# Kernel optimization log

Hardware: AMD Instinct MI355X
Metric: run time of the kernel (lower is better)

## Reference

```python
import jax, jax.numpy as jnp
import numpy as np

B, S, IN, OUT, SPLIT = 4, 2048, 4096, 4096, 1024


def setup_inputs() -> dict:
    key = jax.random.key(0)
    ks = jax.random.split(key, 14)
    def n(k, shape, scale=1.0):
        return jax.random.normal(k, shape, dtype=jnp.float32) * scale
    return {
        "x": n(ks[0], (B, S, IN)),
        "V": n(ks[1], (SPLIT, IN)),
        "U": n(ks[2], (OUT, SPLIT)),
        "v2": n(ks[3], (1, IN), 0.05),
        "v1": n(ks[4], (1, SPLIT), 0.05),
        "u2": n(ks[5], (1, SPLIT), 0.05),
        "u1": n(ks[6], (1, OUT), 0.05),
        "V_R": n(ks[7], (SPLIT, IN)),
        "U_R": n(ks[8], (OUT, SPLIT)),
        "v2_R": n(ks[9], (1, IN), 0.05),
        "v1_R": n(ks[10], (1, SPLIT), 0.05),
        "u2_R": n(ks[11], (1, SPLIT), 0.05),
        "u1_R": n(ks[12], (1, OUT), 0.05),
        "bias": n(ks[13], (OUT,), 0.02),
    }


def _quantize(w):
    # ITQ binarization: sign(w) with straight-through estimator semantics
    return w + jax.lax.stop_gradient(jnp.sign(w) - w)


def _compute_forward(x2d, V, U, v2, v1, u2, u1):
    # x2d: [T, in]; V: [split, in]; U: [out, split]
    Vq = _quantize(V)
    Uq = _quantize(U)
    v1u2 = v1 * u2  # [1, split]
    h = (x2d * v2) @ Vq.T          # [T, split]
    return (h * v1u2) @ Uq.T * u1  # [T, out]


def reference(x, V, U, v2, v1, u2, u1, V_R, U_R, v2_R, v1_R, u2_R, u1_R, bias):
    lead = x.shape[:-1]
    x2d = x.reshape(-1, x.shape[-1])
    y = _compute_forward(x2d, V, U, v2, v1, u2, u1)
    y = y + _compute_forward(x2d, V_R, U_R, v2_R, v1_R, u2_R, u1_R)
    y = y + bias
    return y.reshape(lead + (U.shape[0],))
```

## Files before the change

### kernel.cpp

```cpp
#include <hip/hip_runtime.h>


typedef __bf16 bf16x8 __attribute__((ext_vector_type(8)));
typedef float floatx4 __attribute__((ext_vector_type(4)));

__device__ __forceinline__ unsigned short f2bf_rne(float f) {
    union { float f; unsigned u; } v; v.f = f;
    unsigned r = v.u + 0x7FFFu + ((v.u >> 16) & 1u);
    return (unsigned short)(r >> 16);
}

__device__ __forceinline__ float sgnf(float w) {
    return (float)((w > 0.f) - (w < 0.f));
}

__device__ __forceinline__ void async_copy16(const void* g, void* l) {
    __builtin_amdgcn_global_load_lds(
        (const __attribute__((address_space(1))) void*)g,
        (__attribute__((address_space(3))) void*)l, 16, 0, 0);
}


__global__ void cast_x_kernel(const float* __restrict__ x,
                              unsigned short* __restrict__ xb, int n4) {
    int i = blockIdx.x * blockDim.x + threadIdx.x;
    if (i >= n4) return;
    float4 v = ((const float4*)x)[i];
    ushort4 o;
    o.x = f2bf_rne(v.x); o.y = f2bf_rne(v.y);
    o.z = f2bf_rne(v.z); o.w = f2bf_rne(v.w);
    ((ushort4*)xb)[i] = o;
}

__global__ void prep_w_kernel(const float* __restrict__ V, const float* __restrict__ V_R,
                              const float* __restrict__ v2, const float* __restrict__ v2_R,
                              const float* __restrict__ U, const float* __restrict__ U_R,
                              const float* __restrict__ v1, const float* __restrict__ v1_R,
                              const float* __restrict__ u2, const float* __restrict__ u2_R,
                              const float* __restrict__ u1, const float* __restrict__ u1_R,
                              unsigned short* __restrict__ W1,
                              unsigned short* __restrict__ W2) {
    int bid = blockIdx.x;
    if (bid < 8192) {
        int i = bid * blockDim.x + threadIdx.x;
        int idx = i << 2;
        int scat = idx >> 12;
        int k = idx & 4095;
        const float* Vp; const float* sp;
        if (scat < 1024) { Vp = V + ((size_t)scat << 12); sp = v2; }
        else             { Vp = V_R + ((size_t)(scat - 1024) << 12); sp = v2_R; }
        float4 w = *(const float4*)(Vp + k);
        float4 s = *(const float4*)(sp + k);
        ushort4 o;
        o.x = f2bf_rne(sgnf(w.x) * s.x);
        o.y = f2bf_rne(sgnf(w.y) * s.y);
        o.z = f2bf_rne(sgnf(w.z) * s.z);
        o.w = f2bf_rne(sgnf(w.w) * s.w);
        ((ushort4*)W1)[i] = o;
    } else {
        int i = (bid - 8192) * blockDim.x + threadIdx.x;
        int idx = i << 2;
        int o = idx >> 11;
        int scat = idx & 2047;
        int branch = scat >> 10;
        int s = scat & 1023;
        const float* Up  = branch ? U_R  : U;
        const float* v1p = branch ? v1_R : v1;
        const float* u2p = branch ? u2_R : u2;
        float u1v = (branch ? u1_R : u1)[o];
        float4 w = *(const float4*)(Up + ((size_t)o << 10) + s);
        float4 a = *(const float4*)(v1p + s);
        float4 b = *(const float4*)(u2p + s);
        ushort4 out;
        out.x = f2bf_rne(sgnf(w.x) * a.x * b.x * u1v);
        out.y = f2bf_rne(sgnf(w.y) * a.y * b.y * u1v);
        out.z = f2bf_rne(sgnf(w.z) * a.z * b.z * u1v);
        out.w = f2bf_rne(sgnf(w.w) * a.w * b.w * u1v);
        ((ushort4*)W2)[i] = out;
    }
}


template <bool OUT_BF16, bool ADD_BIAS>
__global__ void gemm_bt(const unsigned short* __restrict__ A,
                        const unsigned short* __restrict__ B,
                        void* __restrict__ Cv,
                        const float* __restrict__ bias,
                        int M, int N, int K) {
    __shared__ __align__(16) unsigned short As[128 * 64];
    __shared__ __align__(16) unsigned short Bs[128 * 64];

    const int tid = threadIdx.x;
    const int wave = tid >> 6;
    const int lane = tid & 63;
    const int m0 = blockIdx.x * 128;
    const int n0 = blockIdx.y * 128;

    const int lrow = lane >> 3;
    const int lcol = (((lane & 7) ^ lrow)) << 3;

    const int wm = (wave >> 1) << 6;
    const int wn = (wave & 1) << 6;
    const int fm = lane & 15;
    const int rk = lane & 7;
    const int cgl = lane >> 4;

    floatx4 acc[4][4];
#pragma unroll
    for (int i = 0; i < 4; ++i)
#pragma unroll
        for (int j = 0; j < 4; ++j)
#pragma unroll
            for (int r = 0; r < 4; ++r) acc[i][j][r] = 0.f;

    const size_t Ks = (size_t)K;
    for (int k0 = 0; k0 < K; k0 += 64) {
#pragma unroll
        for (int i = 0; i < 4; ++i) {
            const int row = wave * 32 + i * 8;
            const unsigned short* gA = A + (size_t)(m0 + row + lrow) * Ks + (k0 + lcol);
            const unsigned short* gB = B + (size_t)(n0 + row + lrow) * Ks + (k0 + lcol);
            async_copy16(gA, &As[row * 64]);
            async_copy16(gB, &Bs[row * 64]);
        }
        __syncthreads();
#pragma unroll
        for (int ks = 0; ks < 64; ks += 32) {
            const int cg = (ks >> 3) | cgl;
            const int roff = (cg ^ rk) << 3;
            bf16x8 af[4], bfr[4];
#pragma unroll
            for (int i = 0; i < 4; ++i)
                af[i] = *(const bf16x8*)&As[(wm + i * 16 + fm) * 64 + roff];
#pragma unroll
            for (int i = 0; i < 4; ++i)
                bfr[i] = *(const bf16x8*)&Bs[(wn + i * 16 + fm) * 64 + roff];
#pragma unroll
            for (int mi = 0; mi < 4; ++mi)
#pragma unroll
                for (int ni = 0; ni < 4; ++ni)
                    acc[mi][ni] = __builtin_amdgcn_mfma_f32_16x16x32_bf16(
                        af[mi], bfr[ni], acc[mi][ni], 0, 0, 0);
        }
        __syncthreads();
    }

    const int rq = (lane >> 4) << 2;
    const int col = lane & 15;
#pragma unroll
    for (int mi = 0; mi < 4; ++mi) {
#pragma unroll
        for (int r = 0; r < 4; ++r) {
            const int gm = m0 + wm + mi * 16 + rq + r;
            const size_t base = (size_t)gm * (size_t)N;
#pragma unroll
            for (int ni = 0; ni < 4; ++ni) {
                const int gn = n0 + wn + ni * 16 + col;
                float v = acc[mi][ni][r];
                if (ADD_BIAS) v += bias[gn];
                if (OUT_BF16)
                    ((unsigned short*)Cv)[base + gn] = f2bf_rne(v);
                else
                    ((float*)Cv)[base + gn] = v;
            }
        }
    }
}


extern "C" void kernel_launch(void* const* d_in, const int* in_sizes, int n_in,
                              void* d_out, int out_size, void* d_ws, size_t ws_size,
                              hipStream_t stream) {
    const float* x    = (const float*)d_in[0];
    const float* V    = (const float*)d_in[1];
    const float* U    = (const float*)d_in[2];
    const float* v2   = (const float*)d_in[3];
    const float* v1   = (const float*)d_in[4];
    const float* u2   = (const float*)d_in[5];
    const float* u1   = (const float*)d_in[6];
    const float* V_R  = (const float*)d_in[7];
    const float* U_R  = (const float*)d_in[8];
    const float* v2_R = (const float*)d_in[9];
    const float* v1_R = (const float*)d_in[10];
    const float* u2_R = (const float*)d_in[11];
    const float* u1_R = (const float*)d_in[12];
    const float* bias = (const float*)d_in[13];
    float* out = (float*)d_out;

    char* ws = (char*)d_ws;
    unsigned short* Xb = (unsigned short*)ws;
    unsigned short* W1 = (unsigned short*)(ws + (size_t)67108864);
    unsigned short* W2 = (unsigned short*)(ws + (size_t)67108864 + 16777216);
    unsigned short* H  = (unsigned short*)(ws + (size_t)67108864 + 33554432);

    cast_x_kernel<<<32768, 256, 0, stream>>>(x, Xb, 8388608);
    prep_w_kernel<<<16384, 256, 0, stream>>>(V, V_R, v2, v2_R,
                                             U, U_R, v1, v1_R, u2, u2_R, u1, u1_R,
                                             W1, W2);

    gemm_bt<true, false><<<dim3(64, 16), 256, 0, stream>>>(Xb, W1, (void*)H, nullptr, 8192, 2048, 4096);
    gemm_bt<false, true><<<dim3(64, 32), 256, 0, stream>>>(H, W2, (void*)out, bias, 8192, 4096, 2048);
}
```

Before: 549.4 us.

## Replace GEMM with 256x256 double-buffered, software-pipelined MFMA kernel

Replaces the 128x128 single-buffered GEMM with a 256x256 tile kernel of 8 waves. It double-buffers LDS, interleaves the async global-to-LDS loads with MFMA quadrants using fine-grained vmcnt waits and barriers, and raises MFMA priority with setprio. It also remaps block IDs with a swizzle for L2 locality. The goal is to hide load latency behind compute and raise arithmetic intensity per tile. The cost is 128KB of LDS per block and high register pressure, which limits occupancy.

```diff
diff --git a/kernel.cpp b/kernel.cpp
--- a/kernel.cpp
+++ b/kernel.cpp
@@ -19,6 +19,10 @@
         (const __attribute__((address_space(1))) void*)g,
         (__attribute__((address_space(3))) void*)l, 16, 0, 0);
 }
+
+#define FENCE() asm volatile("" ::: "memory")
+#define BAR() do { FENCE(); __builtin_amdgcn_s_barrier(); FENCE(); } while (0)
+#define VMW(N) asm volatile("s_waitcnt vmcnt(" #N ")" ::: "memory")
 
 
 __global__ void cast_x_kernel(const float* __restrict__ x,
@@ -82,80 +86,153 @@
 
 
 template <bool OUT_BF16, bool ADD_BIAS>
-__global__ void gemm_bt(const unsigned short* __restrict__ A,
-                        const unsigned short* __restrict__ B,
-                        void* __restrict__ Cv,
-                        const float* __restrict__ bias,
-                        int M, int N, int K) {
-    __shared__ __align__(16) unsigned short As[128 * 64];
-    __shared__ __align__(16) unsigned short Bs[128 * 64];
+__global__ __launch_bounds__(512, 2)
+void gemm256(const unsigned short* __restrict__ A,
+             const unsigned short* __restrict__ B,
+             void* __restrict__ Cv,
+             const float* __restrict__ bias,
+             int M, int N, int K, int ntn) {
+    (void)M;
+    __shared__ __align__(16) unsigned short As[2][256 * 64];
+    __shared__ __align__(16) unsigned short Bs[2][256 * 64];
 
     const int tid = threadIdx.x;
+    const int lane = tid & 63;
     const int wave = tid >> 6;
-    const int lane = tid & 63;
-    const int m0 = blockIdx.x * 128;
-    const int n0 = blockIdx.y * 128;
-
-    const int lrow = lane >> 3;
-    const int lcol = (((lane & 7) ^ lrow)) << 3;
-
-    const int wm = (wave >> 1) << 6;
-    const int wn = (wave & 1) << 6;
+    const int warp_m = wave >> 2;
+    const int warp_n = wave & 3;
+
+    const int nwg = gridDim.x;
+    const int hw = blockIdx.x;
+    const int swz = (hw & 7) * (nwg >> 3) + (hw >> 3);
+    const int tm = swz / ntn;
+    const int tn = swz - tm * ntn;
+    const int m0 = tm << 8;
+    const int n0 = tn << 8;
+
+    const int srow = tid >> 3;
+    const int scg8 = (((tid & 7) ^ (srow & 7)) << 3);
+    const size_t aTB = (size_t)(m0 + srow) * (size_t)K + scg8;
+    const size_t bTB = (size_t)(n0 + srow) * (size_t)K + scg8;
+    const int ldst = tid << 3;
+
+    auto stageA = [&](int buf, int blk, int kt) {
+        async_copy16(A + aTB + ((size_t)(blk << 6)) * (size_t)K + (kt << 6),
+                     &As[buf][(blk << 12) + ldst]);
+    };
+    auto stageB = [&](int buf, int blk, int kt) {
+        async_copy16(B + bTB + ((size_t)(blk << 6)) * (size_t)K + (kt << 6),
+                     &Bs[buf][(blk << 12) + ldst]);
+    };
+
     const int fm = lane & 15;
-    const int rk = lane & 7;
     const int cgl = lane >> 4;
-
-    floatx4 acc[4][4];
-#pragma unroll
-    for (int i = 0; i < 4; ++i)
+    const int key = fm & 7;
+    const int ok0 = ((cgl ^ key) << 3);
+    const int ok1 = (((4 | cgl) ^ key) << 3);
+    const int arow0 = (warp_m << 7) + fm;
+    const int brow0 = (warp_n << 6) + fm;
+
+    auto lda = [&](bf16x8 (&dst)[4][2], int c, int mh) {
+#pragma unroll
+        for (int mi = 0; mi < 4; ++mi) {
+            const unsigned short* p = &As[c][(arow0 + (mh << 6) + (mi << 4)) << 6];
+            dst[mi][0] = *(const bf16x8*)(p + ok0);
+            dst[mi][1] = *(const bf16x8*)(p + ok1);
+        }
+    };
+    auto ldb = [&](bf16x8 (&dst)[2][2], int c, int nh) {
+#pragma unroll
+        for (int ni = 0; ni < 2; ++ni) {
+            const unsigned short* p = &Bs[c][(brow0 + (nh << 5) + (ni << 4)) << 6];
+            dst[ni][0] = *(const bf16x8*)(p + ok0);
+            dst[ni][1] = *(const bf16x8*)(p + ok1);
+        }
+    };
+
+    floatx4 acc[8][4];
+#pragma unroll
+    for (int i = 0; i < 8; ++i)
 #pragma unroll
         for (int j = 0; j < 4; ++j)
 #pragma unroll
             for (int r = 0; r < 4; ++r) acc[i][j][r] = 0.f;
 
-    const size_t Ks = (size_t)K;
-    for (int k0 = 0; k0 < K; k0 += 64) {
-#pragma unroll
-        for (int i = 0; i < 4; ++i) {
-            const int row = wave * 32 + i * 8;
-            const unsigned short* gA = A + (size_t)(m0 + row + lrow) * Ks + (k0 + lcol);
-            const unsigned short* gB = B + (size_t)(n0 + row + lrow) * Ks + (k0 + lcol);
-            async_copy16(gA, &As[row * 64]);
-            async_copy16(gB, &Bs[row * 64]);
-        }
-        __syncthreads();
-#pragma unroll
-        for (int ks = 0; ks < 64; ks += 32) {
-            const int cg = (ks >> 3) | cgl;
-            const int roff = (cg ^ rk) << 3;
-            bf16x8 af[4], bfr[4];
-#pragma unroll
-            for (int i = 0; i < 4; ++i)
-                af[i] = *(const bf16x8*)&As[(wm + i * 16 + fm) * 64 + roff];
-#pragma unroll
-            for (int i = 0; i < 4; ++i)
-                bfr[i] = *(const bf16x8*)&Bs[(wn + i * 16 + fm) * 64 + roff];
-#pragma unroll
-            for (int mi = 0; mi < 4; ++mi)
-#pragma unroll
-                for (int ni = 0; ni < 4; ++ni)
-                    acc[mi][ni] = __builtin_amdgcn_mfma_f32_16x16x32_bf16(
-                        af[mi], bfr[ni], acc[mi][ni], 0, 0, 0);
-        }
-        __syncthreads();
-    }
+    bf16x8 a0[4][2], a1[4][2], b0[2][2], b1[2][2];
+
+#define MMAQ(aS, bS, MH, NH) do { \
+    __builtin_amdgcn_s_setprio(1); \
+    _Pragma("unroll") \
+    for (int mi_ = 0; mi_ < 4; ++mi_) { \
+      _Pragma("unroll") \
+      for (int ni_ = 0; ni_ < 2; ++ni_) { \
+        acc[(MH)*4 + mi_][(NH)*2 + ni_] = __builtin_amdgcn_mfma_f32_16x16x32_bf16( \
+            aS[mi_][0], bS[ni_][0], acc[(MH)*4 + mi_][(NH)*2 + ni_], 0, 0, 0); \
+        acc[(MH)*4 + mi_][(NH)*2 + ni_] = __builtin_amdgcn_mfma_f32_16x16x32_bf16( \
+            aS[mi_][1], bS[ni_][1], acc[(MH)*4 + mi_][(NH)*2 + ni_], 0, 0, 0); \
+      } } \
+    __builtin_amdgcn_s_setprio(0); \
+  } while (0)
+
+#pragma unroll
+    for (int blk = 0; blk < 4; ++blk) stageA(0, blk, 0);
+#pragma unroll
+    for (int blk = 0; blk < 4; ++blk) stageB(0, blk, 0);
+    VMW(0);
+    BAR();
+    lda(a0, 0, 0);
+    ldb(b0, 0, 0);
+
+    const int NT = K >> 6;
+    for (int t = 0; t < NT - 1; ++t) {
+        const int c = t & 1, nc = c ^ 1;
+        stageA(nc, 0, t + 1); stageA(nc, 2, t + 1);
+        stageB(nc, 0, t + 1); stageB(nc, 1, t + 1);
+        stageB(nc, 2, t + 1); stageB(nc, 3, t + 1);
+        ldb(b1, c, 1);
+        MMAQ(a0, b0, 0, 0);
+        VMW(6);
+        BAR();
+        lda(a1, c, 1);
+        MMAQ(a0, b1, 0, 1);
+        VMW(0);
+        BAR();
+        MMAQ(a1, b1, 1, 1);
+        stageA(nc, 1, t + 1); stageA(nc, 3, t + 1);
+        bf16x8 a0n[4][2], b0n[2][2];
+        lda(a0n, nc, 0);
+        ldb(b0n, nc, 0);
+        MMAQ(a1, b0, 1, 0);
+        BAR();
+#pragma unroll
+        for (int mi = 0; mi < 4; ++mi) { a0[mi][0] = a0n[mi][0]; a0[mi][1] = a0n[mi][1]; }
+#pragma unroll
+        for (int ni = 0; ni < 2; ++ni) { b0[ni][0] = b0n[ni][0]; b0[ni][1] = b0n[ni][1]; }
+    }
+    {
+        const int c = (NT - 1) & 1;
+        ldb(b1, c, 1);
+        MMAQ(a0, b0, 0, 0);
+        VMW(0);
+        BAR();
+        lda(a1, c, 1);
+        MMAQ(a0, b1, 0, 1);
+        MMAQ(a1, b1, 1, 1);
+        MMAQ(a1, b0, 1, 0);
+    }
+#undef MMAQ
 
     const int rq = (lane >> 4) << 2;
     const int col = lane & 15;
 #pragma unroll
-    for (int mi = 0; mi < 4; ++mi) {
+    for (int mi = 0; mi < 8; ++mi) {
 #pragma unroll
         for (int r = 0; r < 4; ++r) {
-            const int gm = m0 + wm + mi * 16 + rq + r;
+            const int gm = m0 + (warp_m << 7) + (mi << 4) + rq + r;
             const size_t base = (size_t)gm * (size_t)N;
 #pragma unroll
             for (int ni = 0; ni < 4; ++ni) {
-                const int gn = n0 + wn + ni * 16 + col;
+                const int gn = n0 + (warp_n << 6) + (ni << 4) + col;
                 float v = acc[mi][ni][r];
                 if (ADD_BIAS) v += bias[gn];
                 if (OUT_BF16)
@@ -198,6 +275,8 @@
                                              U, U_R, v1, v1_R, u2, u2_R, u1, u1_R,
                                              W1, W2);
 
-    gemm_bt<true, false><<<dim3(64, 16), 256, 0, stream>>>(Xb, W1, (void*)H, nullptr, 8192, 2048, 4096);
-    gemm_bt<false, true><<<dim3(64, 32), 256, 0, stream>>>(H, W2, (void*)out, bias, 8192, 4096, 2048);
-}
+    gemm256<true, false><<<dim3(256), 512, 0, stream>>>(Xb, W1, (void*)H, nullptr,
+                                                        8192, 2048, 4096, 8);
+    gemm256<false, true><<<dim3(512), 512, 0, stream>>>(H, W2, (void*)out, bias,
+                                                        8192, 4096, 2048, 16);
+}
```

New measurement: 618.0 us. +12.5%, slower.
